# Kernel tuning notes

Measured on AMD Instinct MI355X. Metric: run time of the kernel, lower is better.

The kernel has to match this reference:

```python
import jax, jax.numpy as jnp
import numpy as np


def setup_inputs() -> dict:
    key = jax.random.key(0)
    k1, k2, k3, k4, k5 = jax.random.split(key, 5)
    B, S, DIN, DOUT = 4, 4096, 1024, 4096
    input_ = jax.random.normal(k1, (B, S, DIN), dtype=jnp.float32)
    weights = jax.random.normal(k2, (DOUT, DIN), dtype=jnp.float32) * 0.02
    # two cluster centroids (each shape (1,), as produced by kmeans.cluster_centers_[k])
    c1 = jax.random.uniform(k3, (1,), dtype=jnp.float32) * 0.02
    c2 = -jax.random.uniform(k4, (1,), dtype=jnp.float32) * 0.02
    bias = jax.random.normal(k5, (DOUT,), dtype=jnp.float32) * 0.02
    return {"input_": input_, "weights": weights, "c1": c1, "c2": c2, "bias": bias}


def reference(input_, weights, c1, c2, bias):
    # upper = max(c1, c2), lower = min(c1, c2), threshold = upper - lower
    upper = jnp.maximum(c1, c2)  # (1,)
    lower = jnp.minimum(c1, c2)  # (1,)
    middle = upper - lower       # (1,)
    # binarize weights: w < middle -> lower, else -> upper (fused with GEMM downstream)
    w = jnp.where(weights < middle, lower, upper)  # [DOUT, DIN]
    # F.linear: input @ w.T + bias
    out = jnp.einsum("bsi,oi->bso", input_, w) + bias
    return out
```

## Files before the change

kernel.cpp:

```cpp
#include <hip/hip_runtime.h>
#include <hip/hip_bf16.h>


typedef __bf16 bf16x8 __attribute__((ext_vector_type(8)));
typedef float  f32x4  __attribute__((ext_vector_type(4)));

__device__ inline unsigned short f2bf(float f) {
    unsigned int u = __float_as_uint(f);
    u += 0x7FFFu + ((u >> 16) & 1u);
    return (unsigned short)(u >> 16);
}

__global__ void cvt_x_kernel(const float4* __restrict__ in,
                             ushort4* __restrict__ out, int n4) {
    int stride = gridDim.x * blockDim.x;
    for (int i = blockIdx.x * blockDim.x + threadIdx.x; i < n4; i += stride) {
        float4 v = in[i];
        ushort4 o;
        o.x = f2bf(v.x); o.y = f2bf(v.y); o.z = f2bf(v.z); o.w = f2bf(v.w);
        out[i] = o;
    }
}

__global__ void bin_w_kernel(const float4* __restrict__ w,
                             ushort4* __restrict__ out,
                             const float* __restrict__ c1,
                             const float* __restrict__ c2, int n4) {
    const float a = c1[0], b = c2[0];
    const float upper  = fmaxf(a, b);
    const float lower  = fminf(a, b);
    const float middle = upper - lower;
    const unsigned short lo16 = f2bf(lower);
    const unsigned short up16 = f2bf(upper);
    int stride = gridDim.x * blockDim.x;
    for (int i = blockIdx.x * blockDim.x + threadIdx.x; i < n4; i += stride) {
        float4 v = w[i];
        ushort4 o;
        o.x = (v.x < middle) ? lo16 : up16;
        o.y = (v.y < middle) ? lo16 : up16;
        o.z = (v.z < middle) ? lo16 : up16;
        o.w = (v.w < middle) ? lo16 : up16;
        out[i] = o;
    }
}

__device__ inline void async16(void* lds, const void* g) {
    __builtin_amdgcn_global_load_lds(
        (const __attribute__((address_space(1))) void*)g,
        (__attribute__((address_space(3))) void*)lds,
        16, 0, 0);
}

__global__ __launch_bounds__(256) void gemm_bin(
        const ushort* __restrict__ A,
        const ushort* __restrict__ B,
        const float*  __restrict__ bias,
        float* __restrict__ C,
        int M, int N, int K) {
    __shared__ ushort As[128 * 32];
    __shared__ ushort Bs[128 * 32];

    const int tid  = threadIdx.x;
    const int wave = tid >> 6;
    const int lane = tid & 63;

    const int bn = blockIdx.x;
    const int bm = blockIdx.y;
    const int row0 = bm * 128;
    const int col0 = bn * 128;

    const int wm = (wave & 1) * 64;
    const int wn = (wave >> 1) * 64;

    f32x4 acc[4][4];
#pragma unroll
    for (int i = 0; i < 4; ++i)
#pragma unroll
        for (int j = 0; j < 4; ++j)
            acc[i][j] = (f32x4){0.f, 0.f, 0.f, 0.f};

    const int sr = tid >> 2;
    const int sc = (tid & 3) * 8;
    const ushort* a0 = A + (size_t)(row0 + sr) * K + sc;
    const ushort* a1 = A + (size_t)(row0 + 64 + sr) * K + sc;
    const ushort* b0 = B + (size_t)(col0 + sr) * K + sc;
    const ushort* b1 = B + (size_t)(col0 + 64 + sr) * K + sc;

    ushort* asd0 = &As[wave * 512];
    ushort* asd1 = &As[2048 + wave * 512];
    ushort* bsd0 = &Bs[wave * 512];
    ushort* bsd1 = &Bs[2048 + wave * 512];

    const int fr = lane & 15;
    const int fk = (lane >> 4) * 8;

    for (int k0 = 0; k0 < K; k0 += 32) {
        async16(asd0, a0 + k0);
        async16(asd1, a1 + k0);
        async16(bsd0, b0 + k0);
        async16(bsd1, b1 + k0);
        __syncthreads();

        bf16x8 af[4], bf[4];
#pragma unroll
        for (int i = 0; i < 4; ++i)
            af[i] = *(const bf16x8*)&As[(wm + i * 16 + fr) * 32 + fk];
#pragma unroll
        for (int j = 0; j < 4; ++j)
            bf[j] = *(const bf16x8*)&Bs[(wn + j * 16 + fr) * 32 + fk];

#pragma unroll
        for (int i = 0; i < 4; ++i)
#pragma unroll
            for (int j = 0; j < 4; ++j)
                acc[i][j] = __builtin_amdgcn_mfma_f32_16x16x32_bf16(
                    af[i], bf[j], acc[i][j], 0, 0, 0);

        __syncthreads();
    }

    const int er = (lane >> 4) * 4;
    const int ec = lane & 15;
#pragma unroll
    for (int j = 0; j < 4; ++j) {
        const int col = col0 + wn + j * 16 + ec;
        const float bz = bias[col];
#pragma unroll
        for (int i = 0; i < 4; ++i) {
            const size_t rbase = (size_t)(row0 + wm + i * 16 + er) * N + col;
#pragma unroll
            for (int r = 0; r < 4; ++r)
                C[rbase + (size_t)r * N] = acc[i][j][r] + bz;
        }
    }
}

extern "C" void kernel_launch(void* const* d_in, const int* in_sizes, int n_in,
                              void* d_out, int out_size, void* d_ws, size_t ws_size,
                              hipStream_t stream) {
    const float* x    = (const float*)d_in[0];
    const float* w    = (const float*)d_in[1];
    const float* c1   = (const float*)d_in[2];
    const float* c2   = (const float*)d_in[3];
    const float* bias = (const float*)d_in[4];
    float* out = (float*)d_out;

    const int DOUT = in_sizes[4];
    const int DIN  = in_sizes[1] / DOUT;
    const int M    = in_sizes[0] / DIN;
    const int N    = DOUT;
    const int K    = DIN;

    ushort* xb = (ushort*)d_ws;
    ushort* wb = xb + (size_t)M * K;

    const int nx4 = (M * K) / 4;
    const int nw4 = (N * K) / 4;
    cvt_x_kernel<<<4096, 256, 0, stream>>>((const float4*)x, (ushort4*)xb, nx4);
    bin_w_kernel<<<1024, 256, 0, stream>>>((const float4*)w, (ushort4*)wb, c1, c2, nw4);

    dim3 grid(N / 128, M / 128);
    gemm_bin<<<grid, 256, 0, stream>>>(xb, wb, bias, out, M, N, K);
}
```

Baseline: 474.8 us.

## Rewrite GEMM with 256x256 tiles, multi-stage LDS pipeline, swizzle, and fused prep kernel

Merges the two conversion kernels into a single prep kernel. Rewrites the GEMM to use 256x256 tiles with 8 waves and a 4-slot LDS ring buffer that prefetches two k-steps ahead using async global-to-LDS loads. It also adds an XOR swizzle against LDS bank conflicts, an XCD-aware workgroup remap, split MFMA phases with setprio, and nontemporal output stores. The aim is to hide global load latency and raise data reuse per tile, at the cost of higher register pressure and more complex hand-managed waitcnt synchronisation.

```diff
diff --git a/kernel.cpp b/kernel.cpp
--- a/kernel.cpp
+++ b/kernel.cpp
@@ -11,36 +11,37 @@
     return (unsigned short)(u >> 16);
 }
 
-__global__ void cvt_x_kernel(const float4* __restrict__ in,
-                             ushort4* __restrict__ out, int n4) {
-    int stride = gridDim.x * blockDim.x;
-    for (int i = blockIdx.x * blockDim.x + threadIdx.x; i < n4; i += stride) {
-        float4 v = in[i];
-        ushort4 o;
-        o.x = f2bf(v.x); o.y = f2bf(v.y); o.z = f2bf(v.z); o.w = f2bf(v.w);
-        out[i] = o;
-    }
-}
-
-__global__ void bin_w_kernel(const float4* __restrict__ w,
-                             ushort4* __restrict__ out,
-                             const float* __restrict__ c1,
-                             const float* __restrict__ c2, int n4) {
+__global__ void prep_kernel(const float4* __restrict__ x,
+                            ushort4* __restrict__ xb, int nx4,
+                            const float4* __restrict__ w,
+                            ushort4* __restrict__ wb, int nw4,
+                            const float* __restrict__ c1,
+                            const float* __restrict__ c2) {
     const float a = c1[0], b = c2[0];
     const float upper  = fmaxf(a, b);
     const float lower  = fminf(a, b);
     const float middle = upper - lower;
     const unsigned short lo16 = f2bf(lower);
     const unsigned short up16 = f2bf(upper);
-    int stride = gridDim.x * blockDim.x;
-    for (int i = blockIdx.x * blockDim.x + threadIdx.x; i < n4; i += stride) {
-        float4 v = w[i];
-        ushort4 o;
-        o.x = (v.x < middle) ? lo16 : up16;
-        o.y = (v.y < middle) ? lo16 : up16;
-        o.z = (v.z < middle) ? lo16 : up16;
-        o.w = (v.w < middle) ? lo16 : up16;
-        out[i] = o;
+    const int total  = nx4 + nw4;
+    const int stride = gridDim.x * blockDim.x;
+    for (int i = blockIdx.x * blockDim.x + threadIdx.x; i < total; i += stride) {
+        if (i < nx4) {
+            float4 v = x[i];
+            ushort4 o;
+            o.x = f2bf(v.x); o.y = f2bf(v.y);
+            o.z = f2bf(v.z); o.w = f2bf(v.w);
+            xb[i] = o;
+        } else {
+            const int j = i - nx4;
+            float4 v = w[j];
+            ushort4 o;
+            o.x = (v.x < middle) ? lo16 : up16;
+            o.y = (v.y < middle) ? lo16 : up16;
+            o.z = (v.z < middle) ? lo16 : up16;
+            o.w = (v.w < middle) ? lo16 : up16;
+            wb[j] = o;
+        }
     }
 }
 
@@ -51,72 +52,128 @@
         16, 0, 0);
 }
 
-__global__ __launch_bounds__(256) void gemm_bin(
+#define BAR() do {                                   \
+    asm volatile("" ::: "memory");                   \
+    __builtin_amdgcn_s_barrier();                    \
+    asm volatile("" ::: "memory");                   \
+} while (0)
+
+__global__ __launch_bounds__(512, 2) void gemm_bin(
         const ushort* __restrict__ A,
         const ushort* __restrict__ B,
         const float*  __restrict__ bias,
         float* __restrict__ C,
         int M, int N, int K) {
-    __shared__ ushort As[128 * 32];
-    __shared__ ushort Bs[128 * 32];
+    __shared__ ushort lds[4 * 16384];
 
     const int tid  = threadIdx.x;
     const int wave = tid >> 6;
     const int lane = tid & 63;
 
-    const int bn = blockIdx.x;
-    const int bm = blockIdx.y;
-    const int row0 = bm * 128;
-    const int col0 = bn * 128;
-
-    const int wm = (wave & 1) * 64;
-    const int wn = (wave >> 1) * 64;
-
-    f32x4 acc[4][4];
-#pragma unroll
-    for (int i = 0; i < 4; ++i)
+    const int nwg = gridDim.x;
+    int wg = blockIdx.x;
+    if ((nwg & 7) == 0) {
+        const int cpx = nwg >> 3;
+        wg = (wg & 7) * cpx + (wg >> 3);
+    }
+    const int nbn = N >> 8;
+    const int bm = wg / nbn, bn = wg - bm * nbn;
+    const int row0 = bm << 8, col0 = bn << 8;
+
+    const int wm = (wave >> 2) * 128;
+    const int wn = (wave & 3) * 64;
+
+    const int srow  = wave * 16 + (lane >> 2);
+    const int sulog = (lane & 3) ^ ((srow >> 1) & 3);
+    const ushort* aS0 = A + (size_t)(row0 + srow) * K + sulog * 8;
+    const ushort* aS1 = aS0 + (size_t)128 * K;
+    const ushort* bS0 = B + (size_t)(col0 + srow) * K + sulog * 8;
+    const ushort* bS1 = bS0 + (size_t)128 * K;
+    ushort* const ldsA0 = &lds[        wave * 512];
+    ushort* const ldsA1 = &lds[ 4096 + wave * 512];
+    ushort* const ldsB0 = &lds[ 8192 + wave * 512];
+    ushort* const ldsB1 = &lds[12288 + wave * 512];
+
+    const int fr = lane & 15;
+    const int cu = lane >> 4;
+    const int sw = (fr >> 1) & 3;
+    const int aOff =        (wm + fr) * 32 + ((cu ^ sw) * 8);
+    const int bOff = 8192 + (wn + fr) * 32 + ((cu ^ sw) * 8);
+
+    f32x4 acc[8][4];
+#pragma unroll
+    for (int i = 0; i < 8; ++i)
 #pragma unroll
         for (int j = 0; j < 4; ++j)
             acc[i][j] = (f32x4){0.f, 0.f, 0.f, 0.f};
 
-    const int sr = tid >> 2;
-    const int sc = (tid & 3) * 8;
-    const ushort* a0 = A + (size_t)(row0 + sr) * K + sc;
-    const ushort* a1 = A + (size_t)(row0 + 64 + sr) * K + sc;
-    const ushort* b0 = B + (size_t)(col0 + sr) * K + sc;
-    const ushort* b1 = B + (size_t)(col0 + 64 + sr) * K + sc;
-
-    ushort* asd0 = &As[wave * 512];
-    ushort* asd1 = &As[2048 + wave * 512];
-    ushort* bsd0 = &Bs[wave * 512];
-    ushort* bsd1 = &Bs[2048 + wave * 512];
-
-    const int fr = lane & 15;
-    const int fk = (lane >> 4) * 8;
-
-    for (int k0 = 0; k0 < K; k0 += 32) {
-        async16(asd0, a0 + k0);
-        async16(asd1, a1 + k0);
-        async16(bsd0, b0 + k0);
-        async16(bsd1, b1 + k0);
-        __syncthreads();
+    const int NT = K >> 5;
+
+    async16(ldsA0,         aS0);
+    async16(ldsA1,         aS1);
+    async16(ldsB0,         bS0);
+    async16(ldsB1,         bS1);
+    async16(ldsA0 + 16384, aS0 + 32);
+    async16(ldsA1 + 16384, aS1 + 32);
+    async16(ldsB0 + 16384, bS0 + 32);
+    async16(ldsB1 + 16384, bS1 + 32);
+    asm volatile("s_waitcnt vmcnt(4)" ::: "memory");
+    BAR();
+
+    for (int t = 0; t < NT; ++t) {
+        const int sb = (t & 3) * 16384;
+        const int ss = ((t + 2) & 3) * 16384;
+        const size_t kofs = (size_t)(t + 2) * 32;
+        const bool doStage = (t + 2) < NT;
 
         bf16x8 af[4], bf[4];
-#pragma unroll
-        for (int i = 0; i < 4; ++i)
-            af[i] = *(const bf16x8*)&As[(wm + i * 16 + fr) * 32 + fk];
+
+#pragma unroll
+        for (int i = 0; i < 4; ++i)
+            af[i] = *(const bf16x8*)&lds[sb + aOff + i * 512];
 #pragma unroll
         for (int j = 0; j < 4; ++j)
-            bf[j] = *(const bf16x8*)&Bs[(wn + j * 16 + fr) * 32 + fk];
-
+            bf[j] = *(const bf16x8*)&lds[sb + bOff + j * 512];
+        if (doStage) {
+            async16(ldsA0 + ss, aS0 + kofs);
+            async16(ldsB0 + ss, bS0 + kofs);
+        }
+        BAR();
+        asm volatile("s_waitcnt lgkmcnt(0)" ::: "memory");
+        __builtin_amdgcn_sched_barrier(0);
+        __builtin_amdgcn_s_setprio(1);
 #pragma unroll
         for (int i = 0; i < 4; ++i)
 #pragma unroll
             for (int j = 0; j < 4; ++j)
                 acc[i][j] = __builtin_amdgcn_mfma_f32_16x16x32_bf16(
                     af[i], bf[j], acc[i][j], 0, 0, 0);
-
-        __syncthreads();
+        __builtin_amdgcn_s_setprio(0);
+        BAR();
+
+#pragma unroll
+        for (int i = 0; i < 4; ++i)
+            af[i] = *(const bf16x8*)&lds[sb + aOff + (i + 4) * 512];
+        if (doStage) {
+            async16(ldsA1 + ss, aS1 + kofs);
+            async16(ldsB1 + ss, bS1 + kofs);
+        }
+        if (t < NT - 2)
+            asm volatile("s_waitcnt vmcnt(4)" ::: "memory");
+        else if (t == NT - 2)
+            asm volatile("s_waitcnt vmcnt(0)" ::: "memory");
+        BAR();
+        asm volatile("s_waitcnt lgkmcnt(0)" ::: "memory");
+        __builtin_amdgcn_sched_barrier(0);
+        __builtin_amdgcn_s_setprio(1);
+#pragma unroll
+        for (int i = 0; i < 4; ++i)
+#pragma unroll
+            for (int j = 0; j < 4; ++j)
+                acc[i + 4][j] = __builtin_amdgcn_mfma_f32_16x16x32_bf16(
+                    af[i], bf[j], acc[i + 4][j], 0, 0, 0);
+        __builtin_amdgcn_s_setprio(0);
+        BAR();
     }
 
     const int er = (lane >> 4) * 4;
@@ -126,11 +183,12 @@
         const int col = col0 + wn + j * 16 + ec;
         const float bz = bias[col];
 #pragma unroll
-        for (int i = 0; i < 4; ++i) {
+        for (int i = 0; i < 8; ++i) {
             const size_t rbase = (size_t)(row0 + wm + i * 16 + er) * N + col;
 #pragma unroll
             for (int r = 0; r < 4; ++r)
-                C[rbase + (size_t)r * N] = acc[i][j][r] + bz;
+                __builtin_nontemporal_store(acc[i][j][r] + bz,
+                                            &C[rbase + (size_t)r * N]);
         }
     }
 }
@@ -156,9 +214,10 @@
 
     const int nx4 = (M * K) / 4;
     const int nw4 = (N * K) / 4;
-    cvt_x_kernel<<<4096, 256, 0, stream>>>((const float4*)x, (ushort4*)xb, nx4);
-    bin_w_kernel<<<1024, 256, 0, stream>>>((const float4*)w, (ushort4*)wb, c1, c2, nw4);
-
-    dim3 grid(N / 128, M / 128);
-    gemm_bin<<<grid, 256, 0, stream>>>(xb, wb, bias, out, M, N, K);
-}
+    prep_kernel<<<2048, 256, 0, stream>>>((const float4*)x, (ushort4*)xb, nx4,
+                                          (const float4*)w, (ushort4*)wb, nw4,
+                                          c1, c2);
+
+    dim3 grid((M / 256) * (N / 256));
+    gemm_bin<<<grid, 512, 0, stream>>>(xb, wb, bias, out, M, N, K);
+}
```

New measurement: 450.5 us. 5.1% less time.
